# Kernel optimization log

Hardware: AMD Instinct MI355X
Metric: run time of the kernel (lower is better)

## Reference

```python
import jax, jax.numpy as jnp
import numpy as np

D = 1024      # model_dim
H = 2048      # expert hidden_dim
E = 8         # num routed experts
S = 1         # num shared experts
M = 4         # num modes (1 shared expert per mode)
TOP_K = 2
B, L = 2, 2048


def _ffn(x, w1, b1, w2, b2):
    # x: [T, D]; w1: [..., D, H]; stacked experts via einsum
    h = jnp.einsum('td,edh->teh', x, w1) + b1          # [T, E*, H]
    h = jax.nn.gelu(h)
    return jnp.einsum('teh,ehd->ted', h, w2) + b2      # [T, E*, D]


def setup_inputs() -> dict:
    key = jax.random.key(0)
    ks = jax.random.split(key, 16)
    s = 0.02
    inp = {
        'hidden': jax.random.normal(ks[0], (B, L, D), dtype=jnp.float32),
        'mode_ids': jax.random.randint(ks[1], (B, L), 0, M),
        'router_w': jax.random.normal(ks[2], (D, E), dtype=jnp.float32) * s,
        'router_b': jnp.zeros((E,), dtype=jnp.float32),
        'shared_w1': jax.random.normal(ks[3], (S, D, H), dtype=jnp.float32) * s,
        'shared_b1': jnp.zeros((S, H), dtype=jnp.float32),
        'shared_w2': jax.random.normal(ks[4], (S, H, D), dtype=jnp.float32) * s,
        'shared_b2': jnp.zeros((S, D), dtype=jnp.float32),
        'mode_w1': jax.random.normal(ks[5], (M, D, H), dtype=jnp.float32) * s,
        'mode_b1': jnp.zeros((M, H), dtype=jnp.float32),
        'mode_w2': jax.random.normal(ks[6], (M, H, D), dtype=jnp.float32) * s,
        'mode_b2': jnp.zeros((M, D), dtype=jnp.float32),
        'routed_w1': jax.random.normal(ks[7], (E, D, H), dtype=jnp.float32) * s,
        'routed_b1': jnp.zeros((E, H), dtype=jnp.float32),
        'routed_w2': jax.random.normal(ks[8], (E, H, D), dtype=jnp.float32) * s,
        'routed_b2': jnp.zeros((E, D), dtype=jnp.float32),
    }
    return inp


def reference(hidden, mode_ids, router_w, router_b,
              shared_w1, shared_b1, shared_w2, shared_b2,
              mode_w1, mode_b1, mode_w2, mode_b2,
              routed_w1, routed_b1, routed_w2, routed_b2):
    b, l, d = hidden.shape
    flat = hidden.reshape(b * l, d)                         # [T, D]

    # --- router ---
    router_logits = flat @ router_w + router_b              # [T, E]
    router_probs = jax.nn.softmax(router_logits, axis=-1)
    topk_probs, topk_indices = jax.lax.top_k(router_probs, TOP_K)  # [T, K]

    # --- shared experts (mean over S experts) ---
    shared_out = _ffn(flat, shared_w1, shared_b1, shared_w2, shared_b2).mean(axis=1)  # [T, D]

    # --- mode-conditioned shared experts (1 expert per mode) ---
    mode_flat = mode_ids.reshape(-1)                        # [T]
    mode_onehot = jax.nn.one_hot(mode_flat, M, dtype=flat.dtype)   # [T, M]
    mode_all = _ffn(flat, mode_w1, mode_b1, mode_w2, mode_b2)      # [T, M, D]
    mode_out = jnp.einsum('tm,tmd->td', mode_onehot, mode_all)
    shared_out = shared_out + mode_out

    # --- routed experts: combine weights per (token, expert) ---
    # w[t,e] = sum_k topk_probs[t,k] * (topk_indices[t,k] == e)
    combine_w = jnp.einsum('tke,tk->te',
                           jax.nn.one_hot(topk_indices, E, dtype=flat.dtype),
                           topk_probs)                      # [T, E]
    routed_all = _ffn(flat, routed_w1, routed_b1, routed_w2, routed_b2)  # [T, E, D]
    mixed = jnp.einsum('te,ted->td', combine_w, routed_all)

    output = (shared_out + mixed).reshape(b, l, d)
    aux_logits = router_logits.reshape(b, l, E)
    aux_idx = topk_indices.reshape(b, l, TOP_K)
    aux_probs = topk_probs.reshape(b, l, TOP_K)
    return output, aux_logits, aux_idx, aux_probs
```

## Files before the change

kernel.cpp:

```cpp
#include <hip/hip_runtime.h>
#include <hip/hip_bf16.h>

typedef __hip_bfloat16 bf16t;
using f32x4 = __attribute__((ext_vector_type(4))) float;
using s16x8 = __attribute__((ext_vector_type(8))) short;

#define NTOK 4096
#define DIM 1024
#define HID 2048
#define NEXP 8
#define NMODE 4
#define NGRP 13
#define SLOTS_PAD 16640
#define MAXT 144

static constexpr size_t SZ_WT    = (size_t)NGRP * HID * DIM * 2;
static constexpr size_t OFF_WT1  = 0;
static constexpr size_t OFF_OBUF = 0;
static constexpr size_t OFF_WT2  = OFF_WT1 + SZ_WT;
static constexpr size_t OFF_HBUF = OFF_WT2 + SZ_WT;
static constexpr size_t SZ_HBUF  = (size_t)SLOTS_PAD * HID * 2;
static constexpr size_t OFF_XBF  = OFF_HBUF + SZ_HBUF;
static constexpr size_t SZ_XBF   = (size_t)NTOK * DIM * 2;
static constexpr size_t OFF_B1   = OFF_XBF + SZ_XBF;
static constexpr size_t OFF_B2   = OFF_B1 + (size_t)NGRP * HID * 4;
static constexpr size_t OFF_TP   = OFF_B2 + (size_t)NGRP * DIM * 4;
static constexpr size_t OFF_TI   = OFF_TP + (size_t)NTOK * 2 * 4;
static constexpr size_t OFF_MS   = OFF_TI + (size_t)NTOK * 2 * 4;
static constexpr size_t OFF_R0S  = OFF_MS + (size_t)NTOK * 4;
static constexpr size_t OFF_R1S  = OFF_R0S + (size_t)NTOK * 4;
static constexpr size_t OFF_LIST = OFF_R1S + (size_t)NTOK * 4;
static constexpr size_t OFF_CNT  = OFF_LIST + (size_t)SLOTS_PAD * 4;
static constexpr size_t OFF_CUR  = OFF_CNT + 64;
static constexpr size_t OFF_TC   = OFF_CUR + 64;
static constexpr size_t OFF_TD   = OFF_TC + 16;
static constexpr size_t WS_NEED  = OFF_TD + (size_t)MAXT * 16;

static __device__ __forceinline__ short fb(float f) {
    bf16t h = __float2bfloat16(f);
    short s; __builtin_memcpy(&s, &h, 2); return s;
}
static __device__ __forceinline__ float bf2f(short s) {
    unsigned u = ((unsigned)(unsigned short)s) << 16;
    float f; __builtin_memcpy(&f, &u, 4); return f;
}

static __device__ __forceinline__ float fast_exp(float x) {
#if __has_builtin(__builtin_amdgcn_exp2f)
    return __builtin_amdgcn_exp2f(x * 1.4426950408889634f);
#else
    return exp2f(x * 1.4426950408889634f);
#endif
}
static __device__ __forceinline__ float fast_rcp(float x) {
#if __has_builtin(__builtin_amdgcn_rcpf)
    return __builtin_amdgcn_rcpf(x);
#else
    return 1.0f / x;
#endif
}
static __device__ __forceinline__ float gelu_tanh(float x) {
    float x2 = x * x;
    float u = 0.7978845608028654f * fmaf(0.044715f * x2, x, x);
    u = fminf(u, 15.0f);
    float t = fast_exp(2.0f * u);
    return x * t * fast_rcp(t + 1.0f);
}

typedef __attribute__((address_space(3))) void lds_void;
typedef const __attribute__((address_space(1))) void gbl_void;
static __device__ __forceinline__ void gload16(const void* g, void* l) {
    __builtin_amdgcn_global_load_lds((gbl_void*)g, (lds_void*)l, 16, 0, 0);
}

struct TPtr {
    const float* s_w1; const float* s_w2;
    const float* m_w1; const float* m_w2;
    const float* r_w1; const float* r_w2;
};

static __device__ __forceinline__ void transpose_tile(
    const float* __restrict__ src, bf16t* __restrict__ dst, int R, int C, int x, int y,
    float (*lds)[64][65], int t) {
    const int c0 = x * 64;
    const int ar = t >> 4, ac = (t & 15) * 4;
    const int bc = t >> 3;
    const int rg = (t & 7) * 8;
#pragma unroll
    for (int it = 0; it < 2; ++it) {
        const int r0 = (y * 2 + it) * 64;
#pragma unroll
        for (int p = 0; p < 4; p++) {
            const int r = p * 16 + ar;
            const float4 v = *(const float4*)(src + (size_t)(r0 + r) * C + (c0 + ac));
            lds[it][r][ac] = v.x; lds[it][r][ac + 1] = v.y;
            lds[it][r][ac + 2] = v.z; lds[it][r][ac + 3] = v.w;
        }
    }
    __syncthreads();
#pragma unroll
    for (int it = 0; it < 2; ++it) {
        const int r0 = (y * 2 + it) * 64;
#pragma unroll
        for (int j = 0; j < 2; j++) {
            const int c = j * 32 + bc;
            unsigned w[4];
#pragma unroll
            for (int u = 0; u < 4; u++) {
                unsigned lo = (unsigned short)fb(lds[it][rg + 2 * u][c]);
                unsigned hi = (unsigned short)fb(lds[it][rg + 2 * u + 1][c]);
                w[u] = (hi << 16) | lo;
            }
            *(uint4*)((char*)dst + ((size_t)(c0 + c) * R + (r0 + rg)) * 2) = make_uint4(w[0], w[1], w[2], w[3]);
        }
    }
}

#define TGRID1 3328
#define RGRID  4352
#define PGRID  4456

__global__ __launch_bounds__(256) void prep_k(
    TPtr tp, bf16t* __restrict__ wt1,
    const float* __restrict__ hidden, const int* __restrict__ mode_ids,
    const float* __restrict__ rw, const float* __restrict__ rb,
    float* __restrict__ aux_logits, float* __restrict__ aux_idx, float* __restrict__ aux_probs,
    float* __restrict__ topk_p, int* __restrict__ topk_i, bf16t* __restrict__ xbf,
    const float* __restrict__ sb1, const float* __restrict__ mb1, const float* __restrict__ rb1,
    const float* __restrict__ sb2, const float* __restrict__ mb2, const float* __restrict__ rb2,
    float* __restrict__ B1c, float* __restrict__ B2c) {
    const int bid = blockIdx.x;
    const int t = threadIdx.x;

    if (bid < TGRID1) {
        __shared__ float lds[2][64][65];
        const size_t MSZ = (size_t)DIM * HID;
        const int z = bid >> 8, rem = bid & 255;
        const int x = (rem >> 3) & 31, y = rem & 7;
        const float* src;
        if (z == 0)      src = tp.s_w1;
        else if (z < 5)  src = tp.m_w1 + (size_t)(z - 1) * MSZ;
        else             src = tp.r_w1 + (size_t)(z - 5) * MSZ;
        transpose_tile(src, wt1 + (size_t)z * MSZ, DIM, HID, x, y, lds, t);
        return;
    }

    if (bid < RGRID) {
        const int tok = (bid - TGRID1) * 4 + (t >> 6);
        const int lane = t & 63;
        const float* x = hidden + (size_t)tok * DIM;
        float acc[NEXP];
#pragma unroll
        for (int e = 0; e < NEXP; e++) acc[e] = 0.f;
#pragma unroll
        for (int i = 0; i < DIM / 64; i++) {
            int d = i * 64 + lane;
            float xv = x[d];
            xbf[(size_t)tok * DIM + d] = __float2bfloat16(xv);
            const float4* w = (const float4*)(rw + (size_t)d * NEXP);
            float4 w0 = w[0], w1 = w[1];
            acc[0] += xv * w0.x; acc[1] += xv * w0.y; acc[2] += xv * w0.z; acc[3] += xv * w0.w;
            acc[4] += xv * w1.x; acc[5] += xv * w1.y; acc[6] += xv * w1.z; acc[7] += xv * w1.w;
        }
#pragma unroll
        for (int off = 32; off >= 1; off >>= 1) {
#pragma unroll
            for (int e = 0; e < NEXP; e++) acc[e] += __shfl_down(acc[e], off, 64);
        }
        if (lane == 0) {
            float lg[NEXP], pb[NEXP];
            float mx = -1e30f;
#pragma unroll
            for (int e = 0; e < NEXP; e++) { lg[e] = acc[e] + rb[e]; mx = fmaxf(mx, lg[e]); }
            float s = 0.f;
#pragma unroll
            for (int e = 0; e < NEXP; e++) { pb[e] = expf(lg[e] - mx); s += pb[e]; }
            float inv = 1.f / s;
#pragma unroll
            for (int e = 0; e < NEXP; e++) { pb[e] *= inv; aux_logits[(size_t)tok * NEXP + e] = lg[e]; }
            int i1 = 0;
            for (int e = 1; e < NEXP; e++) if (pb[e] > pb[i1]) i1 = e;
            int i2 = (i1 == 0) ? 1 : 0;
            for (int e = 0; e < NEXP; e++) { if (e == i1) continue; if (pb[e] > pb[i2]) i2 = e; }
            aux_idx[tok * 2] = (float)i1;  aux_idx[tok * 2 + 1] = (float)i2;
            aux_probs[tok * 2] = pb[i1];   aux_probs[tok * 2 + 1] = pb[i2];
            topk_p[tok * 2] = pb[i1];      topk_p[tok * 2 + 1] = pb[i2];
            topk_i[tok * 2] = i1;          topk_i[tok * 2 + 1] = i2;
        }
        return;
    }

    {
        const int i = (bid - RGRID) * 256 + t;
        if (i < NGRP * HID) {
            int g = i / HID, h = i % HID;
            B1c[i] = (g == 0) ? sb1[h] : (g < 5) ? mb1[(g - 1) * HID + h] : rb1[(g - 5) * HID + h];
        }
        if (i < NGRP * DIM) {
            int g = i / DIM, d = i % DIM;
            B2c[i] = (g == 0) ? sb2[d] : (g < 5) ? mb2[(g - 1) * DIM + d] : rb2[(g - 5) * DIM + d];
        }
    }
}

__global__ void count_k(const int* __restrict__ mode_ids, const int* __restrict__ topki,
                        int* __restrict__ cnts) {
    const int lane = threadIdx.x & 63;
    const int wave = threadIdx.x >> 6;
    int local[12];
#pragma unroll
    for (int i = 0; i < 12; i++) local[i] = 0;
    for (int c = blockIdx.x * 4 + wave; c < NTOK / 64; c += 32) {
        const int t = c * 64 + lane;
        const int m  = mode_ids[t];
        const int e0 = topki[t * 2];
        const int e1 = topki[t * 2 + 1];
#pragma unroll
        for (int b = 0; b < 4; b++) local[b] += __popcll(__ballot(m == b));
#pragma unroll
        for (int b = 0; b < 8; b++) {
            local[4 + b] += __popcll(__ballot(e0 == b));
            local[4 + b] += __popcll(__ballot(e1 == b));
        }
    }
    if (lane == 0) {
#pragma unroll
        for (int i = 0; i < 12; i++) atomicAdd(&cnts[i], local[i]);
    }
}

__global__ void scan_k(const int* __restrict__ cnts, int* __restrict__ cursors,
                       int4* __restrict__ tdesc, int* __restrict__ tcount) {
    if (threadIdx.x != 0 || blockIdx.x != 0) return;
    int nt = 0;
    auto emit = [&](int off, int c, int g) {
        for (int r0 = 0; r0 < c; r0 += 128) tdesc[nt++] = make_int4(off + r0, min(128, c - r0), g, 0);
    };
    emit(0, NTOK, 0);
    int off = NTOK;
    for (int m = 0; m < NMODE; m++) { cursors[m] = off; emit(off, cnts[m], 1 + m); off += cnts[m]; }
    off = 2 * NTOK;
    for (int e = 0; e < NEXP; e++) { cursors[NMODE + e] = off; emit(off, cnts[NMODE + e], 5 + e); off += cnts[NMODE + e]; }
    tcount[0] = nt;
}

__global__ void fill_k(const int* __restrict__ mode_ids, const int* __restrict__ topk_i,
                       int* __restrict__ cursors, int* __restrict__ list,
                       int* __restrict__ ms, int* __restrict__ r0s, int* __restrict__ r1s) {
    const int t = blockIdx.x * 256 + threadIdx.x;
    const int lane = threadIdx.x & 63;
    list[t] = t << 1;
    const int m  = mode_ids[t];
    const int e0 = topk_i[t * 2], e1 = topk_i[t * 2 + 1];

    auto put = [&](int bin, bool pred, int payload, int* inv) {
        unsigned long long msk = __ballot(pred);
        if (msk == 0ull) return;
        int leader = __ffsll((unsigned long long)msk) - 1;
        int base = 0;
        if (lane == leader) base = atomicAdd(&cursors[bin], __popcll(msk));
        base = __shfl(base, leader, 64);
        if (pred) {
            int pos = base + __popcll(msk & ((1ull << lane) - 1ull));
            list[pos] = payload;
            inv[t] = pos;
        }
    };
#pragma unroll
    for (int b = 0; b < NMODE; b++) put(b, m == b, t << 1, ms);
#pragma unroll
    for (int b = 0; b < NEXP; b++) put(NMODE + b, e0 == b, t << 1, r0s);
#pragma unroll
    for (int b = 0; b < NEXP; b++) put(NMODE + b, e1 == b, (t << 1) | 1, r1s);
}

#define W2GRID 3328
template <int STAGE>
__global__ __launch_bounds__(256, 3) void ffn_gemm_k(
    const bf16t* __restrict__ xbf,
    const bf16t* __restrict__ hbuf,
    const bf16t* __restrict__ wt,
    const float* __restrict__ bias,
    bf16t* __restrict__ obuf,
    const int* __restrict__ list,
    const int4* __restrict__ tdesc,
    const int* __restrict__ tcount,
    const float* __restrict__ w2s, const float* __restrict__ w2m, const float* __restrict__ w2r,
    bf16t* __restrict__ wt2o) {
    constexpr int K   = (STAGE == 1) ? DIM : HID;
    constexpr int N   = (STAGE == 1) ? HID : DIM;
    constexpr int NK  = K / 32;
    constexpr int NTN = N / 128;
    constexpr int NWG = NTN * MAXT;

    __shared__ alignas(16) char smem[49152];

    if constexpr (STAGE == 1) {
        if (blockIdx.x >= NWG) {
            const int id2 = blockIdx.x - NWG;
            const size_t MSZ = (size_t)DIM * HID;
            const int z = id2 >> 8, rem = id2 & 255;
            const int x = rem >> 4, y = rem & 15;
            const float* src;
            if (z == 0)      src = w2s;
            else if (z < 5)  src = w2m + (size_t)(z - 1) * MSZ;
            else             src = w2r + (size_t)(z - 5) * MSZ;
            transpose_tile(src, wt2o + (size_t)z * MSZ, HID, DIM, x, y,
                           (float (*)[64][65])smem, threadIdx.x);
            return;
        }
    }

    char* As = smem;
    char* Bs = smem + 24576;

    const int lin = blockIdx.x;
    const int wg  = (lin & 7) * (NWG >> 3) + (lin >> 3);
    const int ntile = wg / MAXT;
    const int tix = wg - ntile * MAXT;
    if (tix >= tcount[0]) return;
    const int4 td = tdesc[tix];
    const int slot0 = td.x, rows = td.y, gidx = td.z;
    const int n0 = ntile * 128;

    const int tid  = threadIdx.x;
    const int lane = tid & 63;
    const int w    = tid >> 6;
    const int wm   = w >> 1, wn = w & 1;

    const bf16t* wbase = wt + (size_t)gidx * ((size_t)K * N);
    const bf16t* aP[2];
    const bf16t* bP[2];
#pragma unroll
    for (int h = 0; h < 2; h++) {
        const int r  = (w * 2 + h) * 16 + (lane >> 2);
        const int ce = (((lane & 3) ^ ((r >> 1) & 3)) << 3);
        if (STAGE == 1) aP[h] = xbf + (size_t)(list[slot0 + r] >> 1) * DIM + ce;
        else            aP[h] = hbuf + (size_t)(slot0 + r) * HID + ce;
        bP[h] = wbase + (size_t)(n0 + r) * K + ce;
    }

    auto stage = [&](int t) {
        char* la = As + (t % 3) * 8192 + (w * 2) * 1024 + lane * 16;
        char* lb = Bs + (t % 3) * 8192 + (w * 2) * 1024 + lane * 16;
        gload16(aP[0] + t * 32, la);
        gload16(aP[1] + t * 32, la + 1024);
        gload16(bP[0] + t * 32, lb);
        gload16(bP[1] + t * 32, lb + 1024);
    };

    f32x4 acc[4][4];
    const f32x4 zero = {0.f, 0.f, 0.f, 0.f};
#pragma unroll
    for (int i = 0; i < 4; i++)
#pragma unroll
        for (int j = 0; j < 4; j++) acc[i][j] = zero;

    const int lm = lane & 15;
    const int kc = lane >> 4;

    stage(0); stage(1);

    for (int t = 0; t < NK; ++t) {
        const int cur = t % 3;
        if (t + 1 < NK) asm volatile("s_waitcnt vmcnt(4)" ::: "memory");
        else            asm volatile("s_waitcnt vmcnt(0)" ::: "memory");
        __builtin_amdgcn_s_barrier();

        s16x8 av[4], bv[4];
#pragma unroll
        for (int i = 0; i < 4; i++) {
            const int Ra = wm * 64 + i * 16 + lm;
            av[i] = *(const s16x8*)(As + cur * 8192 + Ra * 64 + ((kc ^ ((Ra >> 1) & 3)) << 4));
            const int Rb = wn * 64 + i * 16 + lm;
            bv[i] = *(const s16x8*)(Bs + cur * 8192 + Rb * 64 + ((kc ^ ((Rb >> 1) & 3)) << 4));
        }
        if (t + 2 < NK) stage(t + 2);

        __builtin_amdgcn_s_setprio(1);
#pragma unroll
        for (int mi = 0; mi < 4; mi++)
#pragma unroll
            for (int ni = 0; ni < 4; ni++)
                acc[mi][ni] = __builtin_amdgcn_mfma_f32_16x16x32_bf16(av[mi], bv[ni], acc[mi][ni], 0, 0, 0);
        __builtin_amdgcn_s_setprio(0);
    }

    const int lr = lane >> 4, lc = lane & 15;
#pragma unroll
    for (int ni = 0; ni < 4; ni++) {
        const int col = n0 + wn * 64 + ni * 16 + lc;
        const float bvv = bias[gidx * N + col];
#pragma unroll
        for (int mi = 0; mi < 4; mi++) {
#pragma unroll
            for (int r = 0; r < 4; r++) {
                const int row = wm * 64 + mi * 16 + lr * 4 + r;
                if (row < rows) {
                    float v = acc[mi][ni][r] + bvv;
                    if (STAGE == 1) v = gelu_tanh(v);
                    obuf[(size_t)(slot0 + row) * N + col] = __float2bfloat16(v);
                }
            }
        }
    }
}

__global__ void reduce_k(const bf16t* __restrict__ ob,
                         const int* __restrict__ ms, const int* __restrict__ r0s, const int* __restrict__ r1s,
                         const float* __restrict__ topkp, float* __restrict__ out) {
    const int t = blockIdx.x * 4 + (threadIdx.x >> 7);
    const int d = (threadIdx.x & 127) * 8;
    const s16x8 a = *(const s16x8*)(ob + (size_t)t * DIM + d);
    const s16x8 b = *(const s16x8*)(ob + (size_t)ms[t] * DIM + d);
    const s16x8 c = *(const s16x8*)(ob + (size_t)r0s[t] * DIM + d);
    const s16x8 e = *(const s16x8*)(ob + (size_t)r1s[t] * DIM + d);
    const float p0 = topkp[t * 2], p1 = topkp[t * 2 + 1];
    float o[8];
#pragma unroll
    for (int j = 0; j < 8; j++)
        o[j] = bf2f(a[j]) + bf2f(b[j]) + p0 * bf2f(c[j]) + p1 * bf2f(e[j]);
    float* dst = out + (size_t)t * DIM + d;
    *(float4*)dst = make_float4(o[0], o[1], o[2], o[3]);
    *(float4*)(dst + 4) = make_float4(o[4], o[5], o[6], o[7]);
}

extern "C" void kernel_launch(void* const* d_in, const int* in_sizes, int n_in,
                              void* d_out, int out_size, void* d_ws, size_t ws_size,
                              hipStream_t stream) {
    (void)in_sizes; (void)n_in; (void)out_size;
    if (ws_size < WS_NEED) return;

    const float* hidden   = (const float*)d_in[0];
    const int*   mode_ids = (const int*)d_in[1];
    const float* router_w = (const float*)d_in[2];
    const float* router_b = (const float*)d_in[3];
    TPtr tp;
    tp.s_w1 = (const float*)d_in[4];
    const float* s_b1 = (const float*)d_in[5];
    tp.s_w2 = (const float*)d_in[6];
    const float* s_b2 = (const float*)d_in[7];
    tp.m_w1 = (const float*)d_in[8];
    const float* m_b1 = (const float*)d_in[9];
    tp.m_w2 = (const float*)d_in[10];
    const float* m_b2 = (const float*)d_in[11];
    tp.r_w1 = (const float*)d_in[12];
    const float* r_b1 = (const float*)d_in[13];
    tp.r_w2 = (const float*)d_in[14];
    const float* r_b2 = (const float*)d_in[15];

    char* ws = (char*)d_ws;
    bf16t* WT1   = (bf16t*)(ws + OFF_WT1);
    bf16t* WT2   = (bf16t*)(ws + OFF_WT2);
    bf16t* Hbuf  = (bf16t*)(ws + OFF_HBUF);
    bf16t* Xbf   = (bf16t*)(ws + OFF_XBF);
    bf16t* Obuf  = (bf16t*)(ws + OFF_OBUF);
    float* B1c   = (float*)(ws + OFF_B1);
    float* B2c   = (float*)(ws + OFF_B2);
    float* topkp = (float*)(ws + OFF_TP);
    int*   topki = (int*)(ws + OFF_TI);
    int*   ms    = (int*)(ws + OFF_MS);
    int*   r0s   = (int*)(ws + OFF_R0S);
    int*   r1s   = (int*)(ws + OFF_R1S);
    int*   list  = (int*)(ws + OFF_LIST);
    int*   cnts  = (int*)(ws + OFF_CNT);
    int*   curs  = (int*)(ws + OFF_CUR);
    int*   tcnt  = (int*)(ws + OFF_TC);
    int4*  td    = (int4*)(ws + OFF_TD);

    float* out        = (float*)d_out;
    float* aux_logits = out + (size_t)NTOK * DIM;
    float* aux_idx    = aux_logits + (size_t)NTOK * NEXP;
    float* aux_probs  = aux_idx + (size_t)NTOK * 2;

    hipMemsetAsync(ws + OFF_LIST, 0, OFF_TC - OFF_LIST, stream);

    prep_k<<<PGRID, 256, 0, stream>>>(tp, WT1,
                                      hidden, mode_ids, router_w, router_b,
                                      aux_logits, aux_idx, aux_probs, topkp, topki, Xbf,
                                      s_b1, m_b1, r_b1, s_b2, m_b2, r_b2, B1c, B2c);
    count_k<<<8, 256, 0, stream>>>(mode_ids, topki, cnts);
    scan_k<<<1, 64, 0, stream>>>(cnts, curs, td, tcnt);
    fill_k<<<NTOK / 256, 256, 0, stream>>>(mode_ids, topki, curs, list, ms, r0s, r1s);
    ffn_gemm_k<1><<<(HID / 128) * MAXT + W2GRID, 256, 0, stream>>>(
        Xbf, Hbuf, WT1, B1c, Hbuf, list, td, tcnt, tp.s_w2, tp.m_w2, tp.r_w2, WT2);
    ffn_gemm_k<2><<<(DIM / 128) * MAXT, 256, 0, stream>>>(
        Xbf, Hbuf, WT2, B2c, Obuf, list, td, tcnt, nullptr, nullptr, nullptr, nullptr);
    reduce_k<<<NTOK / 4, 512, 0, stream>>>(Obuf, ms, r0s, r1s, topkp, out);
}
```

Before: 346.9 us.

## Merge count and scan kernels; shrink GEMM LDS to allow four blocks

Measured after the change: 350.5 us. No clear change (+1.0%).

```diff
diff --git a/kernel.cpp b/kernel.cpp
--- a/kernel.cpp
+++ b/kernel.cpp
@@ -30,8 +30,7 @@
 static constexpr size_t OFF_R0S  = OFF_MS + (size_t)NTOK * 4;
 static constexpr size_t OFF_R1S  = OFF_R0S + (size_t)NTOK * 4;
 static constexpr size_t OFF_LIST = OFF_R1S + (size_t)NTOK * 4;
-static constexpr size_t OFF_CNT  = OFF_LIST + (size_t)SLOTS_PAD * 4;
-static constexpr size_t OFF_CUR  = OFF_CNT + 64;
+static constexpr size_t OFF_CUR  = OFF_LIST + (size_t)SLOTS_PAD * 4;
 static constexpr size_t OFF_TC   = OFF_CUR + 64;
 static constexpr size_t OFF_TD   = OFF_TC + 16;
 static constexpr size_t WS_NEED  = OFF_TD + (size_t)MAXT * 16;
@@ -203,14 +202,21 @@
     }
 }
 
-__global__ void count_k(const int* __restrict__ mode_ids, const int* __restrict__ topki,
-                        int* __restrict__ cnts) {
+__global__ __launch_bounds__(1024) void group_k(
+    const int* __restrict__ mode_ids, const int* __restrict__ topki,
+    int* __restrict__ cursors, int4* __restrict__ tdesc, int* __restrict__ tcount,
+    int* __restrict__ list) {
+    __shared__ int cnts[12];
     const int lane = threadIdx.x & 63;
     const int wave = threadIdx.x >> 6;
+    if (threadIdx.x < 12) cnts[threadIdx.x] = 0;
+    if (threadIdx.x < SLOTS_PAD - 16384) list[16384 + threadIdx.x] = 0;
+    __syncthreads();
     int local[12];
 #pragma unroll
     for (int i = 0; i < 12; i++) local[i] = 0;
-    for (int c = blockIdx.x * 4 + wave; c < NTOK / 64; c += 32) {
+#pragma unroll
+    for (int c = wave; c < NTOK / 64; c += 16) {
         const int t = c * 64 + lane;
         const int m  = mode_ids[t];
         const int e0 = topki[t * 2];
@@ -225,23 +231,21 @@
     }
     if (lane == 0) {
 #pragma unroll
-        for (int i = 0; i < 12; i++) atomicAdd(&cnts[i], local[i]);
-    }
-}
-
-__global__ void scan_k(const int* __restrict__ cnts, int* __restrict__ cursors,
-                       int4* __restrict__ tdesc, int* __restrict__ tcount) {
-    if (threadIdx.x != 0 || blockIdx.x != 0) return;
-    int nt = 0;
-    auto emit = [&](int off, int c, int g) {
-        for (int r0 = 0; r0 < c; r0 += 128) tdesc[nt++] = make_int4(off + r0, min(128, c - r0), g, 0);
-    };
-    emit(0, NTOK, 0);
-    int off = NTOK;
-    for (int m = 0; m < NMODE; m++) { cursors[m] = off; emit(off, cnts[m], 1 + m); off += cnts[m]; }
-    off = 2 * NTOK;
-    for (int e = 0; e < NEXP; e++) { cursors[NMODE + e] = off; emit(off, cnts[NMODE + e], 5 + e); off += cnts[NMODE + e]; }
-    tcount[0] = nt;
+        for (int i = 0; i < 12; i++) if (local[i]) atomicAdd(&cnts[i], local[i]);
+    }
+    __syncthreads();
+    if (threadIdx.x == 0) {
+        int nt = 0;
+        auto emit = [&](int off, int c, int g) {
+            for (int r0 = 0; r0 < c; r0 += 128) tdesc[nt++] = make_int4(off + r0, min(128, c - r0), g, 0);
+        };
+        emit(0, NTOK, 0);
+        int off = NTOK;
+        for (int m = 0; m < NMODE; m++) { cursors[m] = off; emit(off, cnts[m], 1 + m); off += cnts[m]; }
+        off = 2 * NTOK;
+        for (int e = 0; e < NEXP; e++) { cursors[NMODE + e] = off; emit(off, cnts[NMODE + e], 5 + e); off += cnts[NMODE + e]; }
+        tcount[0] = nt;
+    }
 }
 
 __global__ void fill_k(const int* __restrict__ mode_ids, const int* __restrict__ topk_i,
@@ -276,7 +280,7 @@
 
 #define W2GRID 3328
 template <int STAGE>
-__global__ __launch_bounds__(256, 3) void ffn_gemm_k(
+__global__ __launch_bounds__(256, 4) void ffn_gemm_k(
     const bf16t* __restrict__ xbf,
     const bf16t* __restrict__ hbuf,
     const bf16t* __restrict__ wt,
@@ -293,7 +297,7 @@
     constexpr int NTN = N / 128;
     constexpr int NWG = NTN * MAXT;
 
-    __shared__ alignas(16) char smem[49152];
+    __shared__ alignas(16) char smem[40960];
 
     if constexpr (STAGE == 1) {
         if (blockIdx.x >= NWG) {
@@ -312,7 +316,7 @@
     }
 
     char* As = smem;
-    char* Bs = smem + 24576;
+    char* Bs = smem + 16384;
 
     const int lin = blockIdx.x;
     const int wg  = (lin & 7) * (NWG >> 3) + (lin >> 3);
@@ -340,11 +344,13 @@
         bP[h] = wbase + (size_t)(n0 + r) * K + ce;
     }
 
-    auto stage = [&](int t) {
-        char* la = As + (t % 3) * 8192 + (w * 2) * 1024 + lane * 16;
-        char* lb = Bs + (t % 3) * 8192 + (w * 2) * 1024 + lane * 16;
+    auto stageA = [&](int t) {
+        char* la = As + (t & 1) * 8192 + (w * 2) * 1024 + lane * 16;
         gload16(aP[0] + t * 32, la);
         gload16(aP[1] + t * 32, la + 1024);
+    };
+    auto stageB = [&](int t) {
+        char* lb = Bs + (t % 3) * 8192 + (w * 2) * 1024 + lane * 16;
         gload16(bP[0] + t * 32, lb);
         gload16(bP[1] + t * 32, lb + 1024);
     };
@@ -359,11 +365,12 @@
     const int lm = lane & 15;
     const int kc = lane >> 4;
 
-    stage(0); stage(1);
+    stageA(0); stageB(0); stageB(1);
 
     for (int t = 0; t < NK; ++t) {
-        const int cur = t % 3;
-        if (t + 1 < NK) asm volatile("s_waitcnt vmcnt(4)" ::: "memory");
+        const int curA = t & 1;
+        const int curB = t % 3;
+        if (t + 1 < NK) asm volatile("s_waitcnt vmcnt(2)" ::: "memory");
         else            asm volatile("s_waitcnt vmcnt(0)" ::: "memory");
         __builtin_amdgcn_s_barrier();
 
@@ -371,11 +378,12 @@
 #pragma unroll
         for (int i = 0; i < 4; i++) {
             const int Ra = wm * 64 + i * 16 + lm;
-            av[i] = *(const s16x8*)(As + cur * 8192 + Ra * 64 + ((kc ^ ((Ra >> 1) & 3)) << 4));
+            av[i] = *(const s16x8*)(As + curA * 8192 + Ra * 64 + ((kc ^ ((Ra >> 1) & 3)) << 4));
             const int Rb = wn * 64 + i * 16 + lm;
-            bv[i] = *(const s16x8*)(Bs + cur * 8192 + Rb * 64 + ((kc ^ ((Rb >> 1) & 3)) << 4));
-        }
-        if (t + 2 < NK) stage(t + 2);
+            bv[i] = *(const s16x8*)(Bs + curB * 8192 + Rb * 64 + ((kc ^ ((Rb >> 1) & 3)) << 4));
+        }
+        if (t + 1 < NK) stageA(t + 1);
+        if (t + 2 < NK) stageB(t + 2);
 
         __builtin_amdgcn_s_setprio(1);
 #pragma unroll
@@ -463,7 +471,6 @@
     int*   r0s   = (int*)(ws + OFF_R0S);
     int*   r1s   = (int*)(ws + OFF_R1S);
     int*   list  = (int*)(ws + OFF_LIST);
-    int*   cnts  = (int*)(ws + OFF_CNT);
     int*   curs  = (int*)(ws + OFF_CUR);
     int*   tcnt  = (int*)(ws + OFF_TC);
     int4*  td    = (int4*)(ws + OFF_TD);
@@ -473,14 +480,11 @@
     float* aux_idx    = aux_logits + (size_t)NTOK * NEXP;
     float* aux_probs  = aux_idx + (size_t)NTOK * 2;
 
-    hipMemsetAsync(ws + OFF_LIST, 0, OFF_TC - OFF_LIST, stream);
-
     prep_k<<<PGRID, 256, 0, stream>>>(tp, WT1,
                                       hidden, mode_ids, router_w, router_b,
                                       aux_logits, aux_idx, aux_probs, topkp, topki, Xbf,
                                       s_b1, m_b1, r_b1, s_b2, m_b2, r_b2, B1c, B2c);
-    count_k<<<8, 256, 0, stream>>>(mode_ids, topki, cnts);
-    scan_k<<<1, 64, 0, stream>>>(cnts, curs, td, tcnt);
+    group_k<<<1, 1024, 0, stream>>>(mode_ids, topki, curs, td, tcnt, list);
     fill_k<<<NTOK / 256, 256, 0, stream>>>(mode_ids, topki, curs, list, ms, r0s, r1s);
     ffn_gemm_k<1><<<(HID / 128) * MAXT + W2GRID, 256, 0, stream>>>(
         Xbf, Hbuf, WT1, B1c, Hbuf, list, td, tcnt, tp.s_w2, tp.m_w2, tp.r_w2, WT2);
```
